# Kernel tuning notes

Hardware: AMD Instinct MI355X
Metric: run time of the kernel (lower is better)

The kernel has to match this reference:

```python
import jax, jax.numpy as jnp
import numpy as np

DIM_MODEL = 1024
NUM_HEADS = 16
DROPOUT_P = 0.5
SCALE = float(np.sqrt(DIM_MODEL // NUM_HEADS))  # NOTE: source MULTIPLIES by this (unusual but faithful)
DROP_KEY = jax.random.key(42)


def setup_inputs() -> dict:
    key = jax.random.key(0)
    ks = jax.random.split(key, 9)
    B, LQ, LK, D = 4, 2048, 2048, DIM_MODEL
    s = 1.0 / np.sqrt(D)
    return {
        "query": jax.random.normal(ks[0], (B, LQ, D), jnp.float32),
        "key": jax.random.normal(ks[1], (B, LK, D), jnp.float32),
        "value": jax.random.normal(ks[2], (B, LK, D), jnp.float32),
        "Wq": jax.random.normal(ks[3], (D, D), jnp.float32) * s,
        "bq": jax.random.normal(ks[4], (D,), jnp.float32) * s,
        "Wk": jax.random.normal(ks[5], (D, D), jnp.float32) * s,
        "bk": jax.random.normal(ks[6], (D,), jnp.float32) * s,
        "Wv": jax.random.normal(ks[7], (D, D), jnp.float32) * s,
        "bv": jax.random.normal(ks[8], (D,), jnp.float32) * s,
    }


def reference(query, key, value, Wq, bq, Wk, bk, Wv, bv):
    # Linear projections (W stored as [in, out])
    q = jnp.einsum('bqd,de->bqe', query, Wq) + bq
    k = jnp.einsum('bkd,de->bke', key, Wk) + bk
    v = jnp.einsum('bkd,de->bke', value, Wv) + bv
    # scores scaled by MULTIPLYING sqrt(d_head), per source
    scores = jnp.einsum('bqe,bke->bqk', q, k) * SCALE
    probs = jax.nn.softmax(scores, axis=-1)
    # dropout (train mode, p=0.5), deterministic fixed key for reproducibility
    keep = jax.random.bernoulli(DROP_KEY, 1.0 - DROPOUT_P, probs.shape)
    probs = jnp.where(keep, probs / (1.0 - DROPOUT_P), 0.0)
    return jnp.einsum('bqk,bke->bqe', probs, v)
```

## Files before the change

### kernel.cpp

```cpp
#include <hip/hip_runtime.h>
#include <math.h>

#define BATCH  4
#define LSEQ   2048
#define DMODEL 1024
#define MROWS  (BATCH * LSEQ)
#define SCORE_SCALE 8.0f

#define THREEFRY_PARTITIONABLE 1

typedef __bf16 bf16_t;
typedef bf16_t bf16x8 __attribute__((ext_vector_type(8)));
typedef bf16_t bf16x4 __attribute__((ext_vector_type(4)));
typedef float  f32x4  __attribute__((ext_vector_type(4)));

#define LDSP(p) ((__attribute__((address_space(3))) void*)(p))
#define GLBP(p) ((const __attribute__((address_space(1))) void*)(p))

__device__ __forceinline__ unsigned rotl32(unsigned x, int r) {
    return (x << r) | (x >> (32 - r));
}

__device__ __forceinline__ void threefry2x32(unsigned k0, unsigned k1,
                                             unsigned x0, unsigned x1,
                                             unsigned& o0, unsigned& o1) {
    const unsigned ks0 = k0, ks1 = k1, ks2 = k0 ^ k1 ^ 0x1BD11BDAu;
    x0 += ks0; x1 += ks1;
#define TF_R(r) { x0 += x1; x1 = rotl32(x1, r); x1 ^= x0; }
    TF_R(13) TF_R(15) TF_R(26) TF_R(6)
    x0 += ks1; x1 += ks2 + 1u;
    TF_R(17) TF_R(29) TF_R(16) TF_R(24)
    x0 += ks2; x1 += ks0 + 2u;
    TF_R(13) TF_R(15) TF_R(26) TF_R(6)
    x0 += ks0; x1 += ks1 + 3u;
    TF_R(17) TF_R(29) TF_R(16) TF_R(24)
    x0 += ks1; x1 += ks2 + 4u;
    TF_R(13) TF_R(15) TF_R(26) TF_R(6)
    x0 += ks2; x1 += ks0 + 5u;
#undef TF_R
    o0 = x0; o1 = x1;
}

__device__ __forceinline__ bool dropout_keep(unsigned n) {
    unsigned o0, o1;
#if THREEFRY_PARTITIONABLE
    threefry2x32(0u, 42u, 0u, n, o0, o1);
    unsigned bits = o0 ^ o1;
#else
    const unsigned HALF = (unsigned)(BATCH * LSEQ) * (unsigned)LSEQ / 2u;
    unsigned c0 = (n < HALF) ? n : (n - HALF);
    unsigned c1 = (n < HALF) ? (n + HALF) : n;
    threefry2x32(0u, 42u, c0, c1, o0, o1);
    unsigned bits = (n < HALF) ? o0 : o1;
#endif
    return bits < 0x80000000u;
}

__global__ __launch_bounds__(256)
void split_f32(const float* __restrict__ X0, const float* __restrict__ X1,
               bf16_t* __restrict__ hi, bf16_t* __restrict__ lo, int n) {
    const int y = blockIdx.y;
    const float* X = y ? X1 : X0;
    long long i = (long long)(blockIdx.x * 256 + threadIdx.x) * 4;
    if (i >= n) return;
    float4 v = *(const float4*)(X + i);
    bf16x4 h, l;
    h[0] = (bf16_t)v.x; l[0] = (bf16_t)(v.x - (float)h[0]);
    h[1] = (bf16_t)v.y; l[1] = (bf16_t)(v.y - (float)h[1]);
    h[2] = (bf16_t)v.z; l[2] = (bf16_t)(v.z - (float)h[2]);
    h[3] = (bf16_t)v.w; l[3] = (bf16_t)(v.w - (float)h[3]);
    *(bf16x4*)(hi + (long long)y * n + i) = h;
    *(bf16x4*)(lo + (long long)y * n + i) = l;
}

__global__ __launch_bounds__(256)
void cvt_bf16(const float* __restrict__ X, bf16_t* __restrict__ Y, int n) {
    long long i = (long long)(blockIdx.x * 256 + threadIdx.x) * 8;
    if (i >= n) return;
    float4 a = *(const float4*)(X + i);
    float4 b = *(const float4*)(X + i + 4);
    bf16x8 o;
    o[0] = (bf16_t)a.x; o[1] = (bf16_t)a.y; o[2] = (bf16_t)a.z; o[3] = (bf16_t)a.w;
    o[4] = (bf16_t)b.x; o[5] = (bf16_t)b.y; o[6] = (bf16_t)b.z; o[7] = (bf16_t)b.w;
    *(bf16x8*)(Y + i) = o;
}

__global__ __launch_bounds__(256)
void split_transpose(const float* __restrict__ W0, const float* __restrict__ W1,
                     bf16_t* __restrict__ Th, bf16_t* __restrict__ Tl,
                     int Kd, int Nd) {
    __shared__ float t[32][33];
    const int z = blockIdx.z;
    const float* W = z ? W1 : W0;
    const long long zo = (long long)z * Kd * Nd;
    const int bx = blockIdx.x * 32;
    const int by = blockIdx.y * 32;
    const int tx = threadIdx.x & 31, ty = threadIdx.x >> 5;
#pragma unroll
    for (int i = 0; i < 4; ++i)
        t[ty + i * 8][tx] = W[(long long)(by + ty + i * 8) * Nd + bx + tx];
    __syncthreads();
#pragma unroll
    for (int i = 0; i < 4; ++i) {
        float v = t[tx][ty + i * 8];
        long long idx = zo + (long long)(bx + ty + i * 8) * Kd + by + tx;
        bf16_t h = (bf16_t)v;
        Th[idx] = h;
        Tl[idx] = (bf16_t)(v - (float)h);
    }
}

template <int SPLIT, int OUT, int BROW>
__global__ __launch_bounds__(256)
void gemm_mfma(const bf16_t* __restrict__ Ah, const bf16_t* __restrict__ Al,
               const bf16_t* __restrict__ Bh, const bf16_t* __restrict__ Bl,
               const float* __restrict__ bias, const float* __restrict__ bias2,
               float* __restrict__ Cf, bf16_t* __restrict__ Ch,
               bf16_t* __restrict__ Cl,
               int M, int N, int K, float scale,
               long long sA, long long sB, long long sC,
               int SX, int NYt) {
    constexpr int TM = 128, TN = 128, TOT = 256, CHUNKS = 4;
    constexpr int NB = SPLIT ? 2 : 1;
    constexpr int BUFSZ = NB * TOT * 32;
    __shared__ __align__(16) bf16_t smem[2 * BUFSZ];

    const int bid = blockIdx.x;
    const int xcd = bid & 7;
    const int ii = bid >> 3;
    const int perz = SX * NYt;
    const int zz = ii / perz;
    const int rr = ii - zz * perz;
    const int nx = xcd + ((rr % SX) << 3);
    const int my = rr / SX;
    const long long z = zz;
    const int m0 = my * TM, n0 = nx * TN;

    const int tid = threadIdx.x;
    const int lane = tid & 63;
    const int wave = tid >> 6;
    const int quad = lane >> 4;
    const int l16 = lane & 15;
    const int wm = (wave & 1) * 64;
    const int wn = (wave >> 1) * 64;

    const bf16_t* gAh = Ah + z * sA;
    const bf16_t* gBh = Bh + z * sB;
    const bf16_t* gAl = SPLIT ? Al + z * sA : nullptr;
    const bf16_t* gBl = SPLIT ? Bl + z * sB : nullptr;

    const int lrow = lane >> 2;
    const int scol = ((lane & 3) ^ ((lrow >> 1) & 3)) * 8;
    const int sw = (l16 >> 1) & 3;

    auto issue = [&](int k0, int b) {
        bf16_t* base = smem + b * BUFSZ;
#pragma unroll
        for (int c = 0; c < CHUNKS; ++c) {
            const int rbase = wave * 64 + c * 16;
            const int row = rbase + lrow;
            if (rbase < TM) {
                const long long g = (long long)(m0 + row) * K + k0 + scol;
                __builtin_amdgcn_global_load_lds(GLBP(gAh + g), LDSP(base + row * 32), 16, 0, 0);
                if constexpr (SPLIT)
                    __builtin_amdgcn_global_load_lds(GLBP(gAl + g), LDSP(base + TOT * 32 + row * 32), 16, 0, 0);
            } else {
                const int br = row - TM;
                const long long g = (long long)(n0 + br) * K + k0 + scol;
                __builtin_amdgcn_global_load_lds(GLBP(gBh + g), LDSP(base + TM * 32 + br * 32), 16, 0, 0);
                if constexpr (SPLIT)
                    __builtin_amdgcn_global_load_lds(GLBP(gBl + g), LDSP(base + TOT * 32 + TM * 32 + br * 32), 16, 0, 0);
            }
        }
    };

    f32x4 acc[4][4];
#pragma unroll
    for (int i = 0; i < 4; ++i)
#pragma unroll
        for (int j = 0; j < 4; ++j)
            acc[i][j] = (f32x4){0.f, 0.f, 0.f, 0.f};

    issue(0, 0);
    const int NIT = K >> 5;
    for (int it = 0; it < NIT; ++it) {
        const int b = it & 1;
        const bool more = (it + 1) < NIT;
        if (more) issue((it + 1) << 5, b ^ 1);
        if constexpr (SPLIT) {
            if (more) asm volatile("s_waitcnt vmcnt(8)" ::: "memory");
            else      asm volatile("s_waitcnt vmcnt(0)" ::: "memory");
        } else {
            if (more) asm volatile("s_waitcnt vmcnt(4)" ::: "memory");
            else      asm volatile("s_waitcnt vmcnt(0)" ::: "memory");
        }
        asm volatile("s_barrier" ::: "memory");

        bf16_t* base = smem + b * BUFSZ;
        bf16_t* sAh = base;
        bf16_t* sBh = base + TM * 32;
        bf16_t* sAl = base + TOT * 32;
        bf16_t* sBl = base + TOT * 32 + TM * 32;

        bf16x8 afh[4], bfh[4], afl[4], bfl[4];
#pragma unroll
        for (int i = 0; i < 4; ++i) {
            const int ao = (wm + i * 16 + l16) * 32 + (quad ^ sw) * 8;
            afh[i] = *(const bf16x8*)(sAh + ao);
            if constexpr (SPLIT) afl[i] = *(const bf16x8*)(sAl + ao);
        }
#pragma unroll
        for (int j = 0; j < 4; ++j) {
            const int bo = (wn + j * 16 + l16) * 32 + (quad ^ sw) * 8;
            bfh[j] = *(const bf16x8*)(sBh + bo);
            if constexpr (SPLIT) bfl[j] = *(const bf16x8*)(sBl + bo);
        }
#pragma unroll
        for (int i = 0; i < 4; ++i)
#pragma unroll
            for (int j = 0; j < 4; ++j) {
                acc[i][j] = __builtin_amdgcn_mfma_f32_16x16x32_bf16(afh[i], bfh[j], acc[i][j], 0, 0, 0);
                if constexpr (SPLIT) {
                    acc[i][j] = __builtin_amdgcn_mfma_f32_16x16x32_bf16(afh[i], bfl[j], acc[i][j], 0, 0, 0);
                    acc[i][j] = __builtin_amdgcn_mfma_f32_16x16x32_bf16(afl[i], bfh[j], acc[i][j], 0, 0, 0);
                }
            }
        asm volatile("s_barrier" ::: "memory");
    }

    const float* bz = (z == 1 && bias2) ? bias2 : bias;
#pragma unroll
    for (int i = 0; i < 4; ++i)
#pragma unroll
        for (int j = 0; j < 4; ++j) {
            const int n = n0 + wn + j * 16 + l16;
            float bvn = 0.f;
            if constexpr (OUT != 0 && !BROW) bvn = bz[n];
#pragma unroll
            for (int r = 0; r < 4; ++r) {
                const int m = m0 + wm + i * 16 + quad * 4 + r;
                const long long idx = z * sC + (long long)m * N + n;
                float v = acc[i][j][r];
                if constexpr (OUT == 0) {
                    Cf[idx] = v * scale;
                } else if constexpr (OUT == 1) {
                    v += bvn;
                    bf16_t h = (bf16_t)v;
                    Ch[idx] = h;
                    Cl[idx] = (bf16_t)(v - (float)h);
                } else {
                    v += BROW ? bz[m] : bvn;
                    Ch[idx] = (bf16_t)v;
                }
            }
        }
}

template <int OUT>
__global__ __launch_bounds__(512, 2)
void gemm_mfma_8ph(const bf16_t* __restrict__ Ah, const bf16_t* __restrict__ Al,
                   const bf16_t* __restrict__ Bh, const bf16_t* __restrict__ Bl,
                   const float* __restrict__ bias, const float* __restrict__ bias2,
                   float* __restrict__ Cf, bf16_t* __restrict__ Ch,
                   bf16_t* __restrict__ Cl,
                   int M, int N, int K, float scale,
                   long long sA, long long sB, long long sC,
                   int NYt, int NZ) {
    constexpr int TM = 256, TN = 256;
    constexpr int PLANE = 256 * 32;
    __shared__ __align__(16) bf16_t smem[2 * 4 * PLANE];

    const int bid = blockIdx.x;
    const int gid = (bid & 7) * 32 + (bid >> 3);
    const int nzy = NZ * NYt;
    const int nx = gid / nzy;
    const int rem = gid - nx * nzy;
    const int zz = rem / NYt;
    const int my = rem - zz * NYt;
    const long long z = zz;
    const int m0 = my * TM, n0 = nx * TN;

    const int tid = threadIdx.x;
    const int lane = tid & 63;
    const int wave = tid >> 6;
    const int quad = lane >> 4;
    const int l16 = lane & 15;
    const int wm = (wave >> 2) * 128;
    const int wn = (wave & 3) * 64;

    const bf16_t* gAh = Ah + z * sA;
    const bf16_t* gAl = Al + z * sA;
    const bf16_t* gBh = Bh + z * sB;
    const bf16_t* gBl = Bl + z * sB;

    const int lrow = lane >> 2;
    const int scol = ((lane & 3) ^ ((lrow >> 1) & 3)) * 8;
    const int sw = (l16 >> 1) & 3;

    auto stage_round = [&](int r, int k0, int b) {
        bf16_t* base = smem + b * (4 * PLANE);
        if (r < 4) {
            const int row = ((r & 1) << 7) + (wave << 4) + lrow;
            const bf16_t* src = (r >= 2) ? gBl : gBh;
            bf16_t* dst = base + ((r >= 2) ? 3 : 2) * PLANE + row * 32;
            __builtin_amdgcn_global_load_lds(
                GLBP(src + (long long)(n0 + row) * K + k0 + scol), LDSP(dst), 16, 0, 0);
        } else {
            const int p = r - 4;
            const int row = (p << 5) + ((wave & 2) ? 128 : 0) + ((wave & 1) << 4) + lrow;
            const bf16_t* src = (wave >= 4) ? gAl : gAh;
            bf16_t* dst = base + ((wave >= 4) ? 1 : 0) * PLANE + row * 32;
            __builtin_amdgcn_global_load_lds(
                GLBP(src + (long long)(m0 + row) * K + k0 + scol), LDSP(dst), 16, 0, 0);
        }
    };

    f32x4 acc[8][4];
#pragma unroll
    for (int i = 0; i < 8; ++i)
#pragma unroll
        for (int j = 0; j < 4; ++j)
            acc[i][j] = (f32x4){0.f, 0.f, 0.f, 0.f};

#pragma unroll
    for (int r = 0; r < 8; ++r) stage_round(r, 0, 0);
    asm volatile("s_waitcnt vmcnt(3)" ::: "memory");
    asm volatile("s_barrier" ::: "memory");

    const int NIT = K >> 5;
    for (int it = 0; it < NIT; ++it) {
        const int b = it & 1;
        const bool more = (it + 1) < NIT;
        const int k1 = (it + 1) << 5;
        bf16_t* base = smem + b * (4 * PLANE);
        bf16_t* sAh = base;
        bf16_t* sAl = base + PLANE;
        bf16_t* sBh = base + 2 * PLANE;
        bf16_t* sBl = base + 3 * PLANE;

        bf16x8 bfh[4], bfl[4];

#pragma unroll
        for (int ph = 0; ph < 4; ++ph) {
            bf16x8 afh[2], afl[2];
#pragma unroll
            for (int i = 0; i < 2; ++i) {
                const int ao = (wm + (ph * 2 + i) * 16 + l16) * 32 + (quad ^ sw) * 8;
                afh[i] = *(const bf16x8*)(sAh + ao);
                afl[i] = *(const bf16x8*)(sAl + ao);
            }
            if (ph == 0) {
#pragma unroll
                for (int j = 0; j < 4; ++j) {
                    const int bo = (wn + j * 16 + l16) * 32 + (quad ^ sw) * 8;
                    bfh[j] = *(const bf16x8*)(sBh + bo);
                    bfl[j] = *(const bf16x8*)(sBl + bo);
                }
            }

            if (more) {
                stage_round(ph * 2,     k1, b ^ 1);
                stage_round(ph * 2 + 1, k1, b ^ 1);
            }

            if (ph == 0) asm volatile("s_waitcnt lgkmcnt(8)" ::: "memory");
            asm volatile("s_barrier" ::: "memory");
            asm volatile("s_waitcnt lgkmcnt(0)" ::: "memory");
            __builtin_amdgcn_sched_barrier(0);
            __builtin_amdgcn_s_setprio(1);
#pragma unroll
            for (int i = 0; i < 2; ++i)
#pragma unroll
                for (int j = 0; j < 4; ++j) {
                    f32x4 a = acc[ph * 2 + i][j];
                    a = __builtin_amdgcn_mfma_f32_16x16x32_bf16(afh[i], bfh[j], a, 0, 0, 0);
                    a = __builtin_amdgcn_mfma_f32_16x16x32_bf16(afh[i], bfl[j], a, 0, 0, 0);
                    a = __builtin_amdgcn_mfma_f32_16x16x32_bf16(afl[i], bfh[j], a, 0, 0, 0);
                    acc[ph * 2 + i][j] = a;
                }
            __builtin_amdgcn_s_setprio(0);

            if (more) {
                if (ph == 0)      asm volatile("s_waitcnt vmcnt(4)" ::: "memory");
                else if (ph == 1) asm volatile("s_waitcnt vmcnt(5)" ::: "memory");
                else if (ph == 2) asm volatile("s_waitcnt vmcnt(6)" ::: "memory");
                else              asm volatile("s_waitcnt vmcnt(3)" ::: "memory");
            } else {
                if (ph == 0)      asm volatile("s_waitcnt vmcnt(2)" ::: "memory");
                else if (ph == 1) asm volatile("s_waitcnt vmcnt(1)" ::: "memory");
                else if (ph == 2) asm volatile("s_waitcnt vmcnt(0)" ::: "memory");
            }
            asm volatile("s_barrier" ::: "memory");
        }
    }

    const float* bz = (z == 1 && bias2) ? bias2 : bias;
#pragma unroll
    for (int i = 0; i < 8; ++i)
#pragma unroll
        for (int j = 0; j < 4; ++j) {
            const int n = n0 + wn + j * 16 + l16;
            float bvn = 0.f;
            if constexpr (OUT != 0) bvn = bz[n];
#pragma unroll
            for (int r = 0; r < 4; ++r) {
                const int m = m0 + wm + i * 16 + quad * 4 + r;
                const long long idx = z * sC + (long long)m * N + n;
                float v = acc[i][j][r];
                if constexpr (OUT == 0) {
                    Cf[idx] = v * scale;
                } else {
                    v += bvn;
                    bf16_t h = (bf16_t)v;
                    Ch[idx] = h;
                    Cl[idx] = (bf16_t)(v - (float)h);
                }
            }
        }
}

__global__ __launch_bounds__(256)
void softmax_dropout(const float* __restrict__ S, bf16_t* __restrict__ P) {
    const unsigned row = blockIdx.x;
    const float* rp = S + (long long)row * LSEQ;
    const int tid = threadIdx.x;

    float v[8];
    *(float4*)(v)     = *(const float4*)(rp + tid * 8);
    *(float4*)(v + 4) = *(const float4*)(rp + tid * 8 + 4);

    float m = v[0];
#pragma unroll
    for (int e = 1; e < 8; ++e) m = fmaxf(m, v[e]);
#pragma unroll
    for (int o = 1; o < 64; o <<= 1) m = fmaxf(m, __shfl_xor(m, o));
    __shared__ float redm[4];
    if ((tid & 63) == 0) redm[tid >> 6] = m;
    __syncthreads();
    m = fmaxf(fmaxf(redm[0], redm[1]), fmaxf(redm[2], redm[3]));

    float s = 0.f;
#pragma unroll
    for (int e = 0; e < 8; ++e) { v[e] = __expf(v[e] - m); s += v[e]; }
#pragma unroll
    for (int o = 1; o < 64; o <<= 1) s += __shfl_xor(s, o);
    __shared__ float reds[4];
    if ((tid & 63) == 0) reds[tid >> 6] = s;
    __syncthreads();
    s = (reds[0] + reds[1]) + (reds[2] + reds[3]);

    const float inv = 2.0f / s;
    const unsigned nb = row * (unsigned)LSEQ + (unsigned)(tid * 8);
    bf16x8 o8;
#pragma unroll
    for (int e = 0; e < 8; ++e)
        o8[e] = (bf16_t)(dropout_keep(nb + e) ? v[e] * inv : 0.0f);
    *(bf16x8*)(P + (long long)row * LSEQ + tid * 8) = o8;
}

extern "C" void kernel_launch(void* const* d_in, const int* in_sizes, int n_in,
                              void* d_out, int out_size, void* d_ws, size_t ws_size,
                              hipStream_t stream) {
    const float* query = (const float*)d_in[0];
    const float* key_  = (const float*)d_in[1];
    const float* value = (const float*)d_in[2];
    const float* Wq = (const float*)d_in[3];
    const float* bq = (const float*)d_in[4];
    const float* Wk = (const float*)d_in[5];
    const float* bk = (const float*)d_in[6];
    const float* Wv = (const float*)d_in[7];
    const float* bv = (const float*)d_in[8];
    float* out = (float*)d_out;

    char* w = (char*)d_ws;
    const size_t Q1 = (size_t)MROWS * DMODEL * 2;
    bf16_t* Qh  = (bf16_t*)(w);
    bf16_t* Ql  = (bf16_t*)(w + 2 * Q1);
    bf16_t* VT  = (bf16_t*)(w + 4 * Q1);
    float*  S   = (float*)(w + 5 * Q1);
    bf16_t* XvH  = (bf16_t*)(w + 5 * Q1);
    bf16_t* XqkH = (bf16_t*)(w + 5 * Q1);
    bf16_t* XqkL = (bf16_t*)(w + 7 * Q1);
    bf16_t* WTh = (bf16_t*)(w + 9 * Q1);
    bf16_t* WTl = (bf16_t*)(w + 9 * Q1 + 2 * (size_t)DMODEL * DMODEL * 2);
    bf16_t* P   = Qh;

    dim3 b256(256);
    dim3 b512(512);
    const int NELEM = MROWS * DMODEL;
    const long long DD = (long long)DMODEL * DMODEL;
    dim3 gwt1(DMODEL / 32, DMODEL / 32, 1);
    dim3 gwt2(DMODEL / 32, DMODEL / 32, 2);

    split_transpose<<<gwt1, b256, 0, stream>>>(Wv, nullptr, WTh, WTl, DMODEL, DMODEL);
    cvt_bf16<<<dim3(NELEM / 2048), b256, 0, stream>>>(value, XvH, NELEM);
    gemm_mfma<0, 2, 1><<<dim3(512), b256, 0, stream>>>(
        WTh, nullptr, XvH, nullptr, bv, nullptr, nullptr, VT, nullptr,
        DMODEL, LSEQ, DMODEL, 1.f,
        0, (long long)LSEQ * DMODEL, (long long)DMODEL * LSEQ,
        2, DMODEL / 128);

    split_transpose<<<gwt2, b256, 0, stream>>>(Wq, Wk, WTh, WTl, DMODEL, DMODEL);
    split_f32<<<dim3(NELEM / 1024, 2), b256, 0, stream>>>(query, key_, XqkH, XqkL, NELEM);
    gemm_mfma_8ph<1><<<dim3(256), b512, 0, stream>>>(
        XqkH, XqkL, WTh, WTl, bq, bk, nullptr, Qh, Ql,
        MROWS, DMODEL, DMODEL, 1.f,
        (long long)NELEM, DD, (long long)NELEM,
        MROWS / 256, 2);

    gemm_mfma_8ph<0><<<dim3(256), b512, 0, stream>>>(
        Qh, Ql, Qh + NELEM, Ql + NELEM, nullptr, nullptr, S, nullptr, nullptr,
        LSEQ, LSEQ, DMODEL, SCORE_SCALE,
        (long long)LSEQ * DMODEL, (long long)LSEQ * DMODEL,
        (long long)LSEQ * LSEQ,
        LSEQ / 256, 4);

    softmax_dropout<<<dim3(MROWS), b256, 0, stream>>>(S, P);

    gemm_mfma<0, 0, 0><<<dim3(512), b256, 0, stream>>>(
        P, nullptr, VT, nullptr, nullptr, nullptr, out, nullptr, nullptr,
        LSEQ, DMODEL, LSEQ, 1.f,
        (long long)LSEQ * LSEQ, (long long)DMODEL * LSEQ,
        (long long)LSEQ * DMODEL,
        1, LSEQ / 128);
}
```

Baseline: 453.1 us.

## Software-pipeline LDS fragment loads one phase ahead in 8-phase MFMA GEMM

Restructures the GEMM main loop so A fragments for the next phase (and B fragments for the next K-tile) are read from LDS into double-buffered registers while the current phase's MFMAs run. This removes the per-phase lgkmcnt(0) wait before compute. The loop is also unrolled by two with static buffer pointers, and the global_load_lds issue pattern and vmcnt waits are rebalanced. The tradeoffs are higher register pressure from the extra fragment buffers and a greater risk of race hazards from the retuned wait/barrier counts.

```diff
diff --git a/kernel.cpp b/kernel.cpp
--- a/kernel.cpp
+++ b/kernel.cpp
@@ -268,7 +268,8 @@
                    int NYt, int NZ) {
     constexpr int TM = 256, TN = 256;
     constexpr int PLANE = 256 * 32;
-    __shared__ __align__(16) bf16_t smem[2 * 4 * PLANE];
+    constexpr int HB = 4 * PLANE;
+    __shared__ __align__(16) bf16_t smem[2 * HB];
 
     const int bid = blockIdx.x;
     const int gid = (bid & 7) * 32 + (bid >> 3);
@@ -297,8 +298,7 @@
     const int scol = ((lane & 3) ^ ((lrow >> 1) & 3)) * 8;
     const int sw = (l16 >> 1) & 3;
 
-    auto stage_round = [&](int r, int k0, int b) {
-        bf16_t* base = smem + b * (4 * PLANE);
+    auto stage_round = [&](int r, int k0, bf16_t* base) {
         if (r < 4) {
             const int row = ((r & 1) << 7) + (wave << 4) + lrow;
             const bf16_t* src = (r >= 2) ? gBl : gBh;
@@ -322,75 +322,97 @@
         for (int j = 0; j < 4; ++j)
             acc[i][j] = (f32x4){0.f, 0.f, 0.f, 0.f};
 
-#pragma unroll
-    for (int r = 0; r < 8; ++r) stage_round(r, 0, 0);
-    asm volatile("s_waitcnt vmcnt(3)" ::: "memory");
+    bf16x8 ah[2][2], al[2][2];
+    bf16x8 bfh[4], bfl[4];
+
+#pragma unroll
+    for (int r = 0; r < 8; ++r) stage_round(r, 0, smem);
+    asm volatile("s_waitcnt vmcnt(2)" ::: "memory");
     asm volatile("s_barrier" ::: "memory");
+    __builtin_amdgcn_sched_barrier(0);
+#pragma unroll
+    for (int i = 0; i < 2; ++i) {
+        const int ao = (wm + i * 16 + l16) * 32 + (quad ^ sw) * 8;
+        ah[0][i] = *(const bf16x8*)(smem + ao);
+        al[0][i] = *(const bf16x8*)(smem + PLANE + ao);
+    }
+#pragma unroll
+    for (int j = 0; j < 4; ++j) {
+        const int bo = (wn + j * 16 + l16) * 32 + (quad ^ sw) * 8;
+        bfh[j] = *(const bf16x8*)(smem + 2 * PLANE + bo);
+        bfl[j] = *(const bf16x8*)(smem + 3 * PLANE + bo);
+    }
 
     const int NIT = K >> 5;
-    for (int it = 0; it < NIT; ++it) {
-        const int b = it & 1;
-        const bool more = (it + 1) < NIT;
-        const int k1 = (it + 1) << 5;
-        bf16_t* base = smem + b * (4 * PLANE);
-        bf16_t* sAh = base;
-        bf16_t* sAl = base + PLANE;
-        bf16_t* sBh = base + 2 * PLANE;
-        bf16_t* sBl = base + 3 * PLANE;
-
-        bf16x8 bfh[4], bfl[4];
-
-#pragma unroll
-        for (int ph = 0; ph < 4; ++ph) {
-            bf16x8 afh[2], afl[2];
-#pragma unroll
-            for (int i = 0; i < 2; ++i) {
-                const int ao = (wm + (ph * 2 + i) * 16 + l16) * 32 + (quad ^ sw) * 8;
-                afh[i] = *(const bf16x8*)(sAh + ao);
-                afl[i] = *(const bf16x8*)(sAl + ao);
+    for (int itp = 0; itp < NIT; itp += 2) {
+#pragma unroll
+        for (int h = 0; h < 2; ++h) {
+            const int it = itp + h;
+            const bool more = (it + 1) < NIT;
+            const int k1 = (it + 1) << 5;
+            bf16_t* cur = smem + h * HB;
+            bf16_t* nxt = smem + (h ^ 1) * HB;
+#pragma unroll
+            for (int ph = 0; ph < 4; ++ph) {
+                if (ph < 3) {
+#pragma unroll
+                    for (int i = 0; i < 2; ++i) {
+                        const int ao = (wm + ((ph + 1) * 2 + i) * 16 + l16) * 32 + (quad ^ sw) * 8;
+                        ah[(ph + 1) & 1][i] = *(const bf16x8*)(cur + ao);
+                        al[(ph + 1) & 1][i] = *(const bf16x8*)(cur + PLANE + ao);
+                    }
+                } else if (more) {
+#pragma unroll
+                    for (int i = 0; i < 2; ++i) {
+                        const int ao = (wm + i * 16 + l16) * 32 + (quad ^ sw) * 8;
+                        ah[0][i] = *(const bf16x8*)(nxt + ao);
+                        al[0][i] = *(const bf16x8*)(nxt + PLANE + ao);
+                    }
+                }
+                if (more) {
+                    if (ph == 0)      { stage_round(0, k1, nxt); stage_round(1, k1, nxt); stage_round(2, k1, nxt); }
+                    else if (ph == 1) { stage_round(3, k1, nxt); stage_round(4, k1, nxt); }
+                    else if (ph == 2) { stage_round(5, k1, nxt); stage_round(6, k1, nxt); }
+                    else              { stage_round(7, k1, nxt); }
+                }
+                __builtin_amdgcn_s_setprio(1);
+#pragma unroll
+                for (int i = 0; i < 2; ++i)
+#pragma unroll
+                    for (int j = 0; j < 4; ++j) {
+                        f32x4 a = acc[ph * 2 + i][j];
+                        a = __builtin_amdgcn_mfma_f32_16x16x32_bf16(ah[ph & 1][i], bfh[j], a, 0, 0, 0);
+                        a = __builtin_amdgcn_mfma_f32_16x16x32_bf16(ah[ph & 1][i], bfl[j], a, 0, 0, 0);
+                        a = __builtin_amdgcn_mfma_f32_16x16x32_bf16(al[ph & 1][i], bfh[j], a, 0, 0, 0);
+                        acc[ph * 2 + i][j] = a;
+                    }
+                __builtin_amdgcn_s_setprio(0);
+                if (ph == 3 && more) {
+#pragma unroll
+                    for (int j = 0; j < 4; ++j) {
+                        const int bo = (wn + j * 16 + l16) * 32 + (quad ^ sw) * 8;
+                        bfh[j] = *(const bf16x8*)(nxt + 2 * PLANE + bo);
+                        bfl[j] = *(const bf16x8*)(nxt + 3 * PLANE + bo);
+                    }
+                }
+                if (more) {
+                    if (ph == 0)      asm volatile("s_waitcnt vmcnt(4)" ::: "memory");
+                    else if (ph == 1) asm volatile("s_waitcnt vmcnt(5)" ::: "memory");
+                    else              asm volatile("s_waitcnt vmcnt(2)" ::: "memory");
+                    asm volatile("s_barrier" ::: "memory");
+                    __builtin_amdgcn_sched_barrier(0);
+                } else {
+                    if (ph == 0) {
+                        asm volatile("s_waitcnt vmcnt(1)" ::: "memory");
+                        asm volatile("s_barrier" ::: "memory");
+                        __builtin_amdgcn_sched_barrier(0);
+                    } else if (ph == 1) {
+                        asm volatile("s_waitcnt vmcnt(0)" ::: "memory");
+                        asm volatile("s_barrier" ::: "memory");
+                        __builtin_amdgcn_sched_barrier(0);
+                    }
+                }
             }
-            if (ph == 0) {
-#pragma unroll
-                for (int j = 0; j < 4; ++j) {
-                    const int bo = (wn + j * 16 + l16) * 32 + (quad ^ sw) * 8;
-                    bfh[j] = *(const bf16x8*)(sBh + bo);
-                    bfl[j] = *(const bf16x8*)(sBl + bo);
-                }
-            }
-
-            if (more) {
-                stage_round(ph * 2,     k1, b ^ 1);
-                stage_round(ph * 2 + 1, k1, b ^ 1);
-            }
-
-            if (ph == 0) asm volatile("s_waitcnt lgkmcnt(8)" ::: "memory");
-            asm volatile("s_barrier" ::: "memory");
-            asm volatile("s_waitcnt lgkmcnt(0)" ::: "memory");
-            __builtin_amdgcn_sched_barrier(0);
-            __builtin_amdgcn_s_setprio(1);
-#pragma unroll
-            for (int i = 0; i < 2; ++i)
-#pragma unroll
-                for (int j = 0; j < 4; ++j) {
-                    f32x4 a = acc[ph * 2 + i][j];
-                    a = __builtin_amdgcn_mfma_f32_16x16x32_bf16(afh[i], bfh[j], a, 0, 0, 0);
-                    a = __builtin_amdgcn_mfma_f32_16x16x32_bf16(afh[i], bfl[j], a, 0, 0, 0);
-                    a = __builtin_amdgcn_mfma_f32_16x16x32_bf16(afl[i], bfh[j], a, 0, 0, 0);
-                    acc[ph * 2 + i][j] = a;
-                }
-            __builtin_amdgcn_s_setprio(0);
-
-            if (more) {
-                if (ph == 0)      asm volatile("s_waitcnt vmcnt(4)" ::: "memory");
-                else if (ph == 1) asm volatile("s_waitcnt vmcnt(5)" ::: "memory");
-                else if (ph == 2) asm volatile("s_waitcnt vmcnt(6)" ::: "memory");
-                else              asm volatile("s_waitcnt vmcnt(3)" ::: "memory");
-            } else {
-                if (ph == 0)      asm volatile("s_waitcnt vmcnt(2)" ::: "memory");
-                else if (ph == 1) asm volatile("s_waitcnt vmcnt(1)" ::: "memory");
-                else if (ph == 2) asm volatile("s_waitcnt vmcnt(0)" ::: "memory");
-            }
-            asm volatile("s_barrier" ::: "memory");
         }
     }
 
```

Measured after the change: 437.6 us. 1.04x faster.
